# Performance work log

Hardware: AMD Instinct MI355X
Metric: run time of the kernel (lower is better)

## Reference

```python
import jax
import jax.numpy as jnp
import numpy as np

B, T, C = 1024, 512, 32


def setup_inputs() -> dict:
    key = jax.random.key(0)
    k1, k2, k3, k4 = jax.random.split(key, 4)
    pad_x = jax.random.normal(k1, (B, T, C), dtype=jnp.float32)
    transition_scores = jax.random.uniform(k2, (C, C), dtype=jnp.float32)
    origination_scores = jax.random.uniform(k3, (C,), dtype=jnp.float32)
    batch_sizes = jax.random.randint(k4, (B,), 1, T + 1)  # per-sample lengths (unused by the math)
    return {
        "pad_x": pad_x,
        "transition_scores": transition_scores,
        "origination_scores": origination_scores,
        "batch_sizes": batch_sizes,
    }


def reference(pad_x, transition_scores, origination_scores, batch_sizes):
    # CRF forward algorithm (log-space).
    # alpha[0] = emissions[:, 0] + origination
    # alpha[t, b, j] = emissions[b, t, j] + logsumexp_k(alpha[t-1, b, k] + T[j, k])
    alpha0 = pad_x[:, 0, :] + origination_scores[None, :]  # [B, C]
    xs = jnp.swapaxes(pad_x[:, 1:, :], 0, 1)  # time-major [T-1, B, C]

    def step(a_prev, x_t):
        # a_prev: [B, C] (prev tag k); transition_scores: [cur j, prev k]
        scores = a_prev[:, None, :] + transition_scores[None, :, :]  # [B, C, C]
        a_new = x_t + jax.nn.logsumexp(scores, axis=2)  # [B, C]
        return a_new, a_new

    _, rest = jax.lax.scan(step, alpha0, xs)  # rest: [T-1, B, C]
    alpha = jnp.concatenate([alpha0[None], rest], axis=0)  # [T, B, C]
    return alpha
```

## Files before the change

kernel.cpp:

```cpp
#include <hip/hip_runtime.h>
#include <hip/hip_bf16.h>

#define CRF_B 1024
#define CRF_T 512
#define CRF_C 32
#define SEG_S 32
#define SEG_L 16
#define WARM  8

typedef float f32x4 __attribute__((ext_vector_type(4)));
typedef short s16x8 __attribute__((ext_vector_type(8)));

static __device__ __forceinline__ unsigned f2bf(float f) {
    union { float f; unsigned u; } v; v.f = f;
    return (v.u + 0x7FFFu + ((v.u >> 16) & 1u)) >> 16;
}

#define CVT_PK(dst, lo, hi) \
    asm("v_cvt_pk_bf16_f32 %0, %1, %2" : "=v"(dst) : "v"(lo), "v"(hi))
#define SWAP32(a, b) \
    asm("v_permlane32_swap_b32 %0, %1" : "+v"(a), "+v"(b))
#define SWAP16(a, b) \
    asm("v_permlane16_swap_b32 %0, %1" : "+v"(a), "+v"(b))

#define MAKE_AFRAGS()                                                          \
    s16x8 A0, A1;                                                              \
    _Pragma("unroll")                                                          \
    for (int e = 0; e < 8; ++e) {                                              \
        int k_ = h * 8 + e;                                                    \
        A0[e] = (short)f2bf(__expf(trans[r * CRF_C + k_]));                    \
        A1[e] = (short)f2bf(__expf(trans[(16 + r) * CRF_C + k_]));             \
    }

#define LOADSLOT(PL_, PH_, TT_)                                                \
    { const float* pa_ = xb + (size_t)(TT_) * CRF_C;                           \
      PL_ = *(const f32x4*)(pa_ + 4 * h);                                      \
      PH_ = *(const f32x4*)(pa_ + 16 + 4 * h); }

__global__ __launch_bounds__(64) void crf_seam_kernel(
    const float* __restrict__ x, const float* __restrict__ trans,
    const float* __restrict__ orig, float* __restrict__ snap,
    float* __restrict__ ws_u, int CPL)
{
    const int l = threadIdx.x;
    const int r = l & 15;
    const int h = l >> 4;
    const int b = blockIdx.x * 16 + r;
    const int s = blockIdx.y;
    const int zzn = CRF_T / CPL;

    MAKE_AFRAGS();

    const float* xb = x + (size_t)b * CRF_T * CRF_C;
    const int t_a    = (s == 0) ? 0 : (SEG_L * s - WARM);
    const int nsteps = (s == 0) ? (SEG_L - 1) : (SEG_L + WARM - 1);
    const int tend   = t_a + nsteps;

    int kck, zzck, nck;
    if (s == 0) {
        if (CPL == 8) { kck = 7; zzck = 1; nck = 1; }
        else          { kck = 1 << 30; zzck = 0; nck = 0; }
    } else {
        kck = WARM - 1; zzck = s * (SEG_L / CPL); nck = SEG_L / CPL;
    }

    float base0;
    f32x4 ab0, ab1;
    {
        const float* row = xb + (size_t)t_a * CRF_C;
        ab0 = *(const f32x4*)(row + 8 * h);
        ab1 = *(const f32x4*)(row + 8 * h + 4);
        if (s == 0) {
            f32x4 ob0 = *(const f32x4*)(orig + 8 * h);
            f32x4 ob1 = *(const f32x4*)(orig + 8 * h + 4);
            #pragma unroll
            for (int i = 0; i < 4; ++i) { ab0[i] += ob0[i]; ab1[i] += ob1[i]; }
            base0 = row[0] + orig[0];
        } else {
            base0 = row[0];
        }
    }
    float A = base0;
    s16x8 Bf;
    {
        unsigned q0, q1, q2, q3;
        CVT_PK(q0, __expf(ab0[0] - base0), __expf(ab0[1] - base0));
        CVT_PK(q1, __expf(ab0[2] - base0), __expf(ab0[3] - base0));
        CVT_PK(q2, __expf(ab1[0] - base0), __expf(ab1[1] - base0));
        CVT_PK(q3, __expf(ab1[2] - base0), __expf(ab1[3] - base0));
        union { unsigned w[4]; s16x8 v; } bu;
        bu.w[0] = q0; bu.w[1] = q1; bu.w[2] = q2; bu.w[3] = q3;
        Bf = bu.v;
    }

    f32x4 pl0, pl1, pl2, pl3, qh0, qh1, qh2, qh3;
    LOADSLOT(pl0, qh0, t_a + 1) LOADSLOT(pl1, qh1, t_a + 2)
    LOADSLOT(pl2, qh2, t_a + 3) LOADSLOT(pl3, qh3, t_a + 4)

    const f32x4 zz4 = {0.f, 0.f, 0.f, 0.f};
    int t = t_a + 1, k = 1;
    float uval = 0.0f;

#define PSTEP(PL_, PH_)                                                        \
    {                                                                          \
        f32x4 xl = PL_, xh = PH_;                                              \
        { int tn_ = t + 4; if (tn_ > tend) tn_ = tend;                         \
          LOADSLOT(PL_, PH_, tn_) }                                            \
        f32x4 D0 = __builtin_amdgcn_mfma_f32_16x16x32_bf16(A0, Bf, zz4, 0, 0, 0); \
        f32x4 D1 = __builtin_amdgcn_mfma_f32_16x16x32_bf16(A1, Bf, zz4, 0, 0, 0); \
        int ex = (int)((__float_as_uint(D0[0]) >> 23) & 0xFFu) - 127;          \
        ex = __shfl(ex, r, 64);                                                \
        float me = (float)ex;                                                  \
        float Aent = A;                                                        \
        A = Aent + me * 0.69314718055994530942f;                               \
        float f0 = exp2f(fmaf(xl[0], 1.44269504088896f, -me));                 \
        float f1 = exp2f(fmaf(xl[1], 1.44269504088896f, -me));                 \
        float f2 = exp2f(fmaf(xl[2], 1.44269504088896f, -me));                 \
        float f3 = exp2f(fmaf(xl[3], 1.44269504088896f, -me));                 \
        float g0 = exp2f(fmaf(xh[0], 1.44269504088896f, -me));                 \
        float g1 = exp2f(fmaf(xh[1], 1.44269504088896f, -me));                 \
        float g2 = exp2f(fmaf(xh[2], 1.44269504088896f, -me));                 \
        float g3 = exp2f(fmaf(xh[3], 1.44269504088896f, -me));                 \
        if (nck > 0 && k == kck) {   \
            f32x4 vlo, vhi;                                                    \
            vlo[0] = xl[0] + Aent + __logf(D0[0]);                             \
            vlo[1] = xl[1] + Aent + __logf(D0[1]);                             \
            vlo[2] = xl[2] + Aent + __logf(D0[2]);                             \
            vlo[3] = xl[3] + Aent + __logf(D0[3]);                             \
            vhi[0] = xh[0] + Aent + __logf(D1[0]);                             \
            vhi[1] = xh[1] + Aent + __logf(D1[1]);                             \
            vhi[2] = xh[2] + Aent + __logf(D1[2]);                             \
            vhi[3] = xh[3] + Aent + __logf(D1[3]);                             \
            float* vrow = snap + ((size_t)b * zzn + zzck) * CRF_C;             \
            *(f32x4*)(vrow + 4 * h) = vlo;                                     \
            *(f32x4*)(vrow + 16 + 4 * h) = vhi;                                \
            kck += CPL; ++zzck; --nck;                                         \
        }                                                                      \
        if (k == nsteps) uval = xl[0] + Aent + __logf(D0[0]);                  \
        unsigned w0, w1, w2, w3;                                               \
        CVT_PK(w0, D0[0] * f0, D0[1] * f1);                                    \
        CVT_PK(w1, D0[2] * f2, D0[3] * f3);                                    \
        CVT_PK(w2, D1[0] * g0, D1[1] * g1);                                    \
        CVT_PK(w3, D1[2] * g2, D1[3] * g3);                                    \
        SWAP32(w0, w2); SWAP16(w0, w2);                                        \
        SWAP32(w1, w3); SWAP16(w1, w3);                                        \
        {                                                                      \
            union { unsigned w[4]; s16x8 v; } bu_;                             \
            bu_.w[0] = w0; bu_.w[1] = w1; bu_.w[2] = w2; bu_.w[3] = w3;        \
            Bf = bu_.v;                                                        \
        }                                                                      \
        ++t; ++k;                                                              \
    }

    const int ngr = nsteps >> 2;
    for (int g = 0; g < ngr; ++g) {
        PSTEP(pl0, qh0) PSTEP(pl1, qh1) PSTEP(pl2, qh2) PSTEP(pl3, qh3)
    }
    PSTEP(pl0, qh0) PSTEP(pl1, qh1) PSTEP(pl2, qh2)
#undef PSTEP

    if (h == 0) ws_u[(size_t)b * SEG_S + s] = uval;
}

__global__ __launch_bounds__(64) void crf_stitch_kernel(
    const float* __restrict__ snap, const float* __restrict__ ws_u,
    float* __restrict__ ws_c, int CPL)
{
    int b = blockIdx.x * 64 + threadIdx.x;
    const int zzn = CRF_T / CPL, zst = SEG_L / CPL;
    float c = 0.0f;
    ws_c[(size_t)b * SEG_S] = 0.0f;
    for (int s = 1; s < SEG_S; ++s) {
        c += ws_u[(size_t)b * SEG_S + s - 1]
           - snap[((size_t)b * zzn + (size_t)s * zst) * CRF_C];
        ws_c[(size_t)b * SEG_S + s] = c;
    }
}

__global__ __launch_bounds__(64) void crf_out_kernel(
    const float* __restrict__ x, const float* __restrict__ trans,
    const float* __restrict__ orig, const float* __restrict__ snap,
    const float* __restrict__ ws_c, float* __restrict__ out, int CPL)
{
    const int l = threadIdx.x;
    const int r = l & 15;
    const int h = l >> 4;
    const int b = blockIdx.x * 16 + r;
    const int zz = blockIdx.y;
    const int zzn = CRF_T / CPL;

    MAKE_AFRAGS();

    const float* xb = x + (size_t)b * CRF_T * CRF_C;

    int t0, nst;
    float s0;
    s16x8 Bf;
    if (zz == 0) {
        t0 = 1; nst = CPL - 1;
        s0 = xb[0] + orig[0];
        f32x4 ib0 = *(const f32x4*)(xb + 8 * h);
        f32x4 ib1 = *(const f32x4*)(xb + 8 * h + 4);
        f32x4 ob0 = *(const f32x4*)(orig + 8 * h);
        f32x4 ob1 = *(const f32x4*)(orig + 8 * h + 4);
        unsigned q0, q1, q2, q3;
        CVT_PK(q0, __expf(ib0[0] + ob0[0] - s0), __expf(ib0[1] + ob0[1] - s0));
        CVT_PK(q1, __expf(ib0[2] + ob0[2] - s0), __expf(ib0[3] + ob0[3] - s0));
        CVT_PK(q2, __expf(ib1[0] + ob1[0] - s0), __expf(ib1[1] + ob1[1] - s0));
        CVT_PK(q3, __expf(ib1[2] + ob1[2] - s0), __expf(ib1[3] + ob1[3] - s0));
        union { unsigned w[4]; s16x8 v; } bu;
        bu.w[0] = q0; bu.w[1] = q1; bu.w[2] = q2; bu.w[3] = q3;
        Bf = bu.v;
        f32x4 xd0 = *(const f32x4*)(xb + 4 * h);
        f32x4 xd1 = *(const f32x4*)(xb + 16 + 4 * h);
        f32x4 od0 = *(const f32x4*)(orig + 4 * h);
        f32x4 od1 = *(const f32x4*)(orig + 16 + 4 * h);
        f32x4 a00, a01;
        #pragma unroll
        for (int i = 0; i < 4; ++i) { a00[i] = xd0[i] + od0[i]; a01[i] = xd1[i] + od1[i]; }
        *(f32x4*)(out + (size_t)b * CRF_C + 4 * h) = a00;
        *(f32x4*)(out + (size_t)b * CRF_C + 16 + 4 * h) = a01;
    } else {
        t0 = zz * CPL; nst = CPL;
        const int s_seg = (zz * CPL) >> 4;
        const float cc = ws_c[(size_t)b * SEG_S + s_seg];
        const float* vp = snap + ((size_t)b * zzn + zz) * CRF_C;
        const float vp0 = vp[0];
        s0 = vp0 + cc;
        f32x4 vb0 = *(const f32x4*)(vp + 8 * h);
        f32x4 vb1 = *(const f32x4*)(vp + 8 * h + 4);
        unsigned q0, q1, q2, q3;
        CVT_PK(q0, __expf(vb0[0] - vp0), __expf(vb0[1] - vp0));
        CVT_PK(q1, __expf(vb0[2] - vp0), __expf(vb0[3] - vp0));
        CVT_PK(q2, __expf(vb1[0] - vp0), __expf(vb1[1] - vp0));
        CVT_PK(q3, __expf(vb1[2] - vp0), __expf(vb1[3] - vp0));
        union { unsigned w[4]; s16x8 v; } bu;
        bu.w[0] = q0; bu.w[1] = q1; bu.w[2] = q2; bu.w[3] = q3;
        Bf = bu.v;
    }
    const int tendo = zz * CPL + CPL - 1;

    f32x4 pl0, pl1, pl2, pl3, qh0, qh1, qh2, qh3;
    LOADSLOT(pl0, qh0, t0)     LOADSLOT(pl1, qh1, t0 + 1)
    LOADSLOT(pl2, qh2, t0 + 2) LOADSLOT(pl3, qh3, t0 + 3)

    const f32x4 zz4 = {0.f, 0.f, 0.f, 0.f};
    float sU = s0, sC = s0, aQ = s0;
    float* op0 = out + ((size_t)t0 * CRF_B + b) * CRF_C + 4 * h;
    int t = t0;

#define STEP(PL_, PH_)                                                         \
    {                                                                          \
        f32x4 xl = PL_, xh = PH_;                                              \
        { int tn_ = t + 4; if (tn_ > tendo) tn_ = tendo;                       \
          LOADSLOT(PL_, PH_, tn_) }                                            \
        f32x4 D0 = __builtin_amdgcn_mfma_f32_16x16x32_bf16(A0, Bf, zz4, 0, 0, 0); \
        f32x4 D1 = __builtin_amdgcn_mfma_f32_16x16x32_bf16(A1, Bf, zz4, 0, 0, 0); \
        float dlt = sU - sC;                                                   \
        float f0 = __expf(xl[0] + dlt), f1 = __expf(xl[1] + dlt);              \
        float f2 = __expf(xl[2] + dlt), f3 = __expf(xl[3] + dlt);              \
        float g0 = __expf(xh[0] + dlt), g1 = __expf(xh[1] + dlt);              \
        float g2 = __expf(xh[2] + dlt), g3 = __expf(xh[3] + dlt);              \
        f32x4 alo, ahi;                                                        \
        alo[0] = xl[0] + sU + __logf(D0[0]);                                   \
        alo[1] = xl[1] + sU + __logf(D0[1]);                                   \
        alo[2] = xl[2] + sU + __logf(D0[2]);                                   \
        alo[3] = xl[3] + sU + __logf(D0[3]);                                   \
        ahi[0] = xh[0] + sU + __logf(D1[0]);                                   \
        ahi[1] = xh[1] + sU + __logf(D1[1]);                                   \
        ahi[2] = xh[2] + sU + __logf(D1[2]);                                   \
        ahi[3] = xh[3] + sU + __logf(D1[3]);                                   \
        *(f32x4*)op0 = alo;                                                    \
        *(f32x4*)(op0 + 16) = ahi;                                             \
        op0 += (size_t)CRF_B * CRF_C;                                          \
        float a0new = __shfl(alo[0], r, 64);                                   \
        unsigned w0, w1, w2, w3;                                               \
        CVT_PK(w0, D0[0] * f0, D0[1] * f1);                                    \
        CVT_PK(w1, D0[2] * f2, D0[3] * f3);                                    \
        CVT_PK(w2, D1[0] * g0, D1[1] * g1);                                    \
        CVT_PK(w3, D1[2] * g2, D1[3] * g3);                                    \
        SWAP32(w0, w2); SWAP16(w0, w2);                                        \
        SWAP32(w1, w3); SWAP16(w1, w3);                                        \
        {                                                                      \
            union { unsigned w[4]; s16x8 v; } bu_;                             \
            bu_.w[0] = w0; bu_.w[1] = w1; bu_.w[2] = w2; bu_.w[3] = w3;        \
            Bf = bu_.v;                                                        \
        }                                                                      \
        sU = sC; sC = aQ; aQ = a0new;                                          \
        ++t;                                                                   \
    }

    const int ngr = nst >> 2;
    for (int g = 0; g < ngr; ++g) {
        STEP(pl0, qh0) STEP(pl1, qh1) STEP(pl2, qh2) STEP(pl3, qh3)
    }
    if (nst & 3) {
        STEP(pl0, qh0) STEP(pl1, qh1) STEP(pl2, qh2)
    }
#undef STEP
}

__global__ __launch_bounds__(64) void crf_fwd_fallback(
    const float* __restrict__ x, const float* __restrict__ trans,
    const float* __restrict__ orig, float* __restrict__ out)
{
    const int l = threadIdx.x;
    const int r = l & 15;
    const int h = l >> 4;
    const int b = blockIdx.x * 16 + r;

    MAKE_AFRAGS();

    const float* xb = x + (size_t)b * CRF_T * CRF_C;
    float s0 = xb[0] + orig[0];

    f32x4 ib0 = *(const f32x4*)(xb + 8 * h);
    f32x4 ib1 = *(const f32x4*)(xb + 8 * h + 4);
    f32x4 ob0 = *(const f32x4*)(orig + 8 * h);
    f32x4 ob1 = *(const f32x4*)(orig + 8 * h + 4);
    unsigned q0, q1, q2, q3;
    CVT_PK(q0, __expf(ib0[0] + ob0[0] - s0), __expf(ib0[1] + ob0[1] - s0));
    CVT_PK(q1, __expf(ib0[2] + ob0[2] - s0), __expf(ib0[3] + ob0[3] - s0));
    CVT_PK(q2, __expf(ib1[0] + ob1[0] - s0), __expf(ib1[1] + ob1[1] - s0));
    CVT_PK(q3, __expf(ib1[2] + ob1[2] - s0), __expf(ib1[3] + ob1[3] - s0));
    s16x8 Bf;
    {
        union { unsigned w[4]; s16x8 v; } bu;
        bu.w[0] = q0; bu.w[1] = q1; bu.w[2] = q2; bu.w[3] = q3;
        Bf = bu.v;
    }
    {
        f32x4 xd0 = *(const f32x4*)(xb + 4 * h);
        f32x4 xd1 = *(const f32x4*)(xb + 16 + 4 * h);
        f32x4 od0 = *(const f32x4*)(orig + 4 * h);
        f32x4 od1 = *(const f32x4*)(orig + 16 + 4 * h);
        f32x4 a00, a01;
        #pragma unroll
        for (int i = 0; i < 4; ++i) { a00[i] = xd0[i] + od0[i]; a01[i] = xd1[i] + od1[i]; }
        *(f32x4*)(out + (size_t)b * CRF_C + 4 * h) = a00;
        *(f32x4*)(out + (size_t)b * CRF_C + 16 + 4 * h) = a01;
    }

    f32x4 pl0, pl1, pl2, pl3, qh0, qh1, qh2, qh3;
    LOADSLOT(pl0, qh0, 1) LOADSLOT(pl1, qh1, 2)
    LOADSLOT(pl2, qh2, 3) LOADSLOT(pl3, qh3, 4)

    const f32x4 zz4 = {0.f, 0.f, 0.f, 0.f};
    float sU = s0, sC = s0, aQ = s0;
    float* op0 = out + ((size_t)CRF_B + b) * CRF_C + 4 * h;
    int t = 1;

#define STEP(PL_, PH_)                                                         \
    {                                                                          \
        f32x4 xl = PL_, xh = PH_;                                              \
        { int tn_ = t + 4; if (tn_ > CRF_T - 1) tn_ = CRF_T - 1;               \
          LOADSLOT(PL_, PH_, tn_) }                                            \
        f32x4 D0 = __builtin_amdgcn_mfma_f32_16x16x32_bf16(A0, Bf, zz4, 0, 0, 0); \
        f32x4 D1 = __builtin_amdgcn_mfma_f32_16x16x32_bf16(A1, Bf, zz4, 0, 0, 0); \
        float dlt = sU - sC;                                                   \
        float f0 = __expf(xl[0] + dlt), f1 = __expf(xl[1] + dlt);              \
        float f2 = __expf(xl[2] + dlt), f3 = __expf(xl[3] + dlt);              \
        float g0 = __expf(xh[0] + dlt), g1 = __expf(xh[1] + dlt);              \
        float g2 = __expf(xh[2] + dlt), g3 = __expf(xh[3] + dlt);              \
        f32x4 alo, ahi;                                                        \
        alo[0] = xl[0] + sU + __logf(D0[0]);                                   \
        alo[1] = xl[1] + sU + __logf(D0[1]);                                   \
        alo[2] = xl[2] + sU + __logf(D0[2]);                                   \
        alo[3] = xl[3] + sU + __logf(D0[3]);                                   \
        ahi[0] = xh[0] + sU + __logf(D1[0]);                                   \
        ahi[1] = xh[1] + sU + __logf(D1[1]);                                   \
        ahi[2] = xh[2] + sU + __logf(D1[2]);                                   \
        ahi[3] = xh[3] + sU + __logf(D1[3]);                                   \
        *(f32x4*)op0 = alo;                                                    \
        *(f32x4*)(op0 + 16) = ahi;                                             \
        op0 += (size_t)CRF_B * CRF_C;                                          \
        float a0new = __shfl(alo[0], r, 64);                                   \
        unsigned w0, w1, w2, w3;                                               \
        CVT_PK(w0, D0[0] * f0, D0[1] * f1);                                    \
        CVT_PK(w1, D0[2] * f2, D0[3] * f3);                                    \
        CVT_PK(w2, D1[0] * g0, D1[1] * g1);                                    \
        CVT_PK(w3, D1[2] * g2, D1[3] * g3);                                    \
        SWAP32(w0, w2); SWAP16(w0, w2);                                        \
        SWAP32(w1, w3); SWAP16(w1, w3);                                        \
        {                                                                      \
            union { unsigned w[4]; s16x8 v; } bu_;                             \
            bu_.w[0] = w0; bu_.w[1] = w1; bu_.w[2] = w2; bu_.w[3] = w3;        \
            Bf = bu_.v;                                                        \
        }                                                                      \
        sU = sC; sC = aQ; aQ = a0new;                                          \
        ++t;                                                                   \
    }

    for (int g = 0; g < 127; ++g) {
        STEP(pl0, qh0) STEP(pl1, qh1) STEP(pl2, qh2) STEP(pl3, qh3)
    }
    STEP(pl0, qh0) STEP(pl1, qh1) STEP(pl2, qh2)
#undef STEP
}

extern "C" void kernel_launch(void* const* d_in, const int* in_sizes, int n_in,
                              void* d_out, int out_size, void* d_ws, size_t ws_size,
                              hipStream_t stream) {
    const float* pad_x = (const float*)d_in[0];
    const float* trans = (const float*)d_in[1];
    const float* orig  = (const float*)d_in[2];
    float* out = (float*)d_out;

    const size_t uc_bytes = (size_t)CRF_B * SEG_S * sizeof(float);
    const size_t snap8  = (size_t)CRF_B * 64 * CRF_C * sizeof(float);
    const size_t snap16 = (size_t)CRF_B * 32 * CRF_C * sizeof(float);

    int CPL = 0;
    if (ws_size >= snap8 + 2 * uc_bytes)       CPL = 8;
    else if (ws_size >= snap16 + 2 * uc_bytes) CPL = 16;

    if (CPL == 0) {
        crf_fwd_fallback<<<dim3(CRF_B / 16), dim3(64), 0, stream>>>(
            pad_x, trans, orig, out);
        return;
    }
    const int zzn = CRF_T / CPL;
    float* snap = (float*)d_ws;
    float* ws_u = snap + (size_t)CRF_B * zzn * CRF_C;
    float* ws_c = ws_u + (size_t)CRF_B * SEG_S;

    crf_seam_kernel<<<dim3(CRF_B / 16, SEG_S), dim3(64), 0, stream>>>(
        pad_x, trans, orig, snap, ws_u, CPL);
    crf_stitch_kernel<<<dim3(CRF_B / 64), dim3(64), 0, stream>>>(
        snap, ws_u, ws_c, CPL);
    crf_out_kernel<<<dim3(CRF_B / 16, zzn), dim3(64), 0, stream>>>(
        pad_x, trans, orig, snap, ws_c, out, CPL);
}
```

Before: 55.29 us.

## Template segment length and fold stitch prefix-sum into the output kernel

Segment length becomes a template parameter (8 or 16), so the seam kernel runs one segment per output chunk with a fixed warm-up. Each seam block writes a single snapshot instead of tracking several checkpoints. The separate stitch kernel is removed: each output block recomputes the cumulative offset for its segment with a serial loop over earlier segments. This drops one launch and its global round-trip, and with SL=8 it doubles the number of seam segments. The cost is more redundant warm-up steps, plus an O(s) prefix loop of global reads in every output block.

```diff
diff --git a/kernel.cpp b/kernel.cpp
--- a/kernel.cpp
+++ b/kernel.cpp
@@ -4,8 +4,6 @@
 #define CRF_B 1024
 #define CRF_T 512
 #define CRF_C 32
-#define SEG_S 32
-#define SEG_L 16
 #define WARM  8
 
 typedef float f32x4 __attribute__((ext_vector_type(4)));
@@ -37,32 +35,25 @@
       PL_ = *(const f32x4*)(pa_ + 4 * h);                                      \
       PH_ = *(const f32x4*)(pa_ + 16 + 4 * h); }
 
+template <int SL>
 __global__ __launch_bounds__(64) void crf_seam_kernel(
     const float* __restrict__ x, const float* __restrict__ trans,
     const float* __restrict__ orig, float* __restrict__ snap,
-    float* __restrict__ ws_u, int CPL)
+    float* __restrict__ uu)
 {
+    const int SEG_S = CRF_T / SL;
     const int l = threadIdx.x;
     const int r = l & 15;
     const int h = l >> 4;
     const int b = blockIdx.x * 16 + r;
     const int s = blockIdx.y;
-    const int zzn = CRF_T / CPL;
 
     MAKE_AFRAGS();
 
     const float* xb = x + (size_t)b * CRF_T * CRF_C;
-    const int t_a    = (s == 0) ? 0 : (SEG_L * s - WARM);
-    const int nsteps = (s == 0) ? (SEG_L - 1) : (SEG_L + WARM - 1);
+    const int t_a    = (s == 0) ? 0 : (SL * s - WARM);
+    const int nsteps = (s == 0) ? (SL - 1) : (SL + WARM - 1);
     const int tend   = t_a + nsteps;
-
-    int kck, zzck, nck;
-    if (s == 0) {
-        if (CPL == 8) { kck = 7; zzck = 1; nck = 1; }
-        else          { kck = 1 << 30; zzck = 0; nck = 0; }
-    } else {
-        kck = WARM - 1; zzck = s * (SEG_L / CPL); nck = SEG_L / CPL;
-    }
 
     float base0;
     f32x4 ab0, ab1;
@@ -100,6 +91,7 @@
     const f32x4 zz4 = {0.f, 0.f, 0.f, 0.f};
     int t = t_a + 1, k = 1;
     float uval = 0.0f;
+    float* vrow = snap + ((size_t)b * SEG_S + s) * CRF_C;
 
 #define PSTEP(PL_, PH_)                                                        \
     {                                                                          \
@@ -121,7 +113,7 @@
         float g1 = exp2f(fmaf(xh[1], 1.44269504088896f, -me));                 \
         float g2 = exp2f(fmaf(xh[2], 1.44269504088896f, -me));                 \
         float g3 = exp2f(fmaf(xh[3], 1.44269504088896f, -me));                 \
-        if (nck > 0 && k == kck) {   \
+        if ((s != 0) && (k == WARM - 1)) {     \
             f32x4 vlo, vhi;                                                    \
             vlo[0] = xl[0] + Aent + __logf(D0[0]);                             \
             vlo[1] = xl[1] + Aent + __logf(D0[1]);                             \
@@ -131,10 +123,8 @@
             vhi[1] = xh[1] + Aent + __logf(D1[1]);                             \
             vhi[2] = xh[2] + Aent + __logf(D1[2]);                             \
             vhi[3] = xh[3] + Aent + __logf(D1[3]);                             \
-            float* vrow = snap + ((size_t)b * zzn + zzck) * CRF_C;             \
             *(f32x4*)(vrow + 4 * h) = vlo;                                     \
             *(f32x4*)(vrow + 16 + 4 * h) = vhi;                                \
-            kck += CPL; ++zzck; --nck;                                         \
         }                                                                      \
         if (k == nsteps) uval = xl[0] + Aent + __logf(D0[0]);                  \
         unsigned w0, w1, w2, w3;                                               \
@@ -159,35 +149,21 @@
     PSTEP(pl0, qh0) PSTEP(pl1, qh1) PSTEP(pl2, qh2)
 #undef PSTEP
 
-    if (h == 0) ws_u[(size_t)b * SEG_S + s] = uval;
+    if (h == 0) uu[(size_t)b * SEG_S + s] = uval;
 }
 
-__global__ __launch_bounds__(64) void crf_stitch_kernel(
-    const float* __restrict__ snap, const float* __restrict__ ws_u,
-    float* __restrict__ ws_c, int CPL)
-{
-    int b = blockIdx.x * 64 + threadIdx.x;
-    const int zzn = CRF_T / CPL, zst = SEG_L / CPL;
-    float c = 0.0f;
-    ws_c[(size_t)b * SEG_S] = 0.0f;
-    for (int s = 1; s < SEG_S; ++s) {
-        c += ws_u[(size_t)b * SEG_S + s - 1]
-           - snap[((size_t)b * zzn + (size_t)s * zst) * CRF_C];
-        ws_c[(size_t)b * SEG_S + s] = c;
-    }
-}
-
+template <int SL>
 __global__ __launch_bounds__(64) void crf_out_kernel(
     const float* __restrict__ x, const float* __restrict__ trans,
     const float* __restrict__ orig, const float* __restrict__ snap,
-    const float* __restrict__ ws_c, float* __restrict__ out, int CPL)
+    const float* __restrict__ uu, float* __restrict__ out)
 {
+    const int SEG_S = CRF_T / SL;
     const int l = threadIdx.x;
     const int r = l & 15;
     const int h = l >> 4;
     const int b = blockIdx.x * 16 + r;
-    const int zz = blockIdx.y;
-    const int zzn = CRF_T / CPL;
+    const int s = blockIdx.y;
 
     MAKE_AFRAGS();
 
@@ -196,8 +172,8 @@
     int t0, nst;
     float s0;
     s16x8 Bf;
-    if (zz == 0) {
-        t0 = 1; nst = CPL - 1;
+    if (s == 0) {
+        t0 = 1; nst = SL - 1;
         s0 = xb[0] + orig[0];
         f32x4 ib0 = *(const f32x4*)(xb + 8 * h);
         f32x4 ib1 = *(const f32x4*)(xb + 8 * h + 4);
@@ -221,12 +197,14 @@
         *(f32x4*)(out + (size_t)b * CRF_C + 4 * h) = a00;
         *(f32x4*)(out + (size_t)b * CRF_C + 16 + 4 * h) = a01;
     } else {
-        t0 = zz * CPL; nst = CPL;
-        const int s_seg = (zz * CPL) >> 4;
-        const float cc = ws_c[(size_t)b * SEG_S + s_seg];
-        const float* vp = snap + ((size_t)b * zzn + zz) * CRF_C;
+        t0 = SL * s; nst = SL;
+        float c = 0.0f;
+        for (int sp = 1; sp <= s; ++sp)
+            c += uu[(size_t)b * SEG_S + sp - 1]
+               - snap[((size_t)b * SEG_S + sp) * CRF_C];
+        const float* vp = snap + ((size_t)b * SEG_S + s) * CRF_C;
         const float vp0 = vp[0];
-        s0 = vp0 + cc;
+        s0 = vp0 + c;
         f32x4 vb0 = *(const f32x4*)(vp + 8 * h);
         f32x4 vb1 = *(const f32x4*)(vp + 8 * h + 4);
         unsigned q0, q1, q2, q3;
@@ -238,7 +216,7 @@
         bu.w[0] = q0; bu.w[1] = q1; bu.w[2] = q2; bu.w[3] = q3;
         Bf = bu.v;
     }
-    const int tendo = zz * CPL + CPL - 1;
+    const int tendo = SL * s + SL - 1;
 
     f32x4 pl0, pl1, pl2, pl3, qh0, qh1, qh2, qh3;
     LOADSLOT(pl0, qh0, t0)     LOADSLOT(pl1, qh1, t0 + 1)
@@ -406,28 +384,28 @@
     const float* orig  = (const float*)d_in[2];
     float* out = (float*)d_out;
 
-    const size_t uc_bytes = (size_t)CRF_B * SEG_S * sizeof(float);
-    const size_t snap8  = (size_t)CRF_B * 64 * CRF_C * sizeof(float);
-    const size_t snap16 = (size_t)CRF_B * 32 * CRF_C * sizeof(float);
-
-    int CPL = 0;
-    if (ws_size >= snap8 + 2 * uc_bytes)       CPL = 8;
-    else if (ws_size >= snap16 + 2 * uc_bytes) CPL = 16;
-
-    if (CPL == 0) {
+    auto need = [](int SL) {
+        return (size_t)CRF_B * (CRF_T / SL) * (CRF_C + 1) * sizeof(float);
+    };
+
+    if (ws_size >= need(8)) {
+        const int SEG_S = CRF_T / 8;
+        float* snap = (float*)d_ws;
+        float* uu   = snap + (size_t)CRF_B * SEG_S * CRF_C;
+        crf_seam_kernel<8><<<dim3(CRF_B / 16, SEG_S), dim3(64), 0, stream>>>(
+            pad_x, trans, orig, snap, uu);
+        crf_out_kernel<8><<<dim3(CRF_B / 16, SEG_S), dim3(64), 0, stream>>>(
+            pad_x, trans, orig, snap, uu, out);
+    } else if (ws_size >= need(16)) {
+        const int SEG_S = CRF_T / 16;
+        float* snap = (float*)d_ws;
+        float* uu   = snap + (size_t)CRF_B * SEG_S * CRF_C;
+        crf_seam_kernel<16><<<dim3(CRF_B / 16, SEG_S), dim3(64), 0, stream>>>(
+            pad_x, trans, orig, snap, uu);
+        crf_out_kernel<16><<<dim3(CRF_B / 16, SEG_S), dim3(64), 0, stream>>>(
+            pad_x, trans, orig, snap, uu, out);
+    } else {
         crf_fwd_fallback<<<dim3(CRF_B / 16), dim3(64), 0, stream>>>(
             pad_x, trans, orig, out);
-        return;
-    }
-    const int zzn = CRF_T / CPL;
-    float* snap = (float*)d_ws;
-    float* ws_u = snap + (size_t)CRF_B * zzn * CRF_C;
-    float* ws_c = ws_u + (size_t)CRF_B * SEG_S;
-
-    crf_seam_kernel<<<dim3(CRF_B / 16, SEG_S), dim3(64), 0, stream>>>(
-        pad_x, trans, orig, snap, ws_u, CPL);
-    crf_stitch_kernel<<<dim3(CRF_B / 64), dim3(64), 0, stream>>>(
-        snap, ws_u, ws_c, CPL);
-    crf_out_kernel<<<dim3(CRF_B / 16, zzn), dim3(64), 0, stream>>>(
-        pad_x, trans, orig, snap, ws_c, out, CPL);
+    }
 }
```

Result: slower. 76.54 us (+38.4%).
